# Kernel tuning notes

Hardware: AMD Instinct MI355X
Metric: run time of the kernel (lower is better)

## Reference

```python
import jax, jax.numpy as jnp
import numpy as np

N, C, H, W, D = 4, 320, 16, 16, 16
POS_RATIO = 0.5


def setup_inputs() -> dict:
    key = jax.random.key(0)
    k1, k2, k3, k4 = jax.random.split(key, 4)
    q = jax.random.normal(k1, (N, C, H, W, D), jnp.float32)
    k = jax.random.normal(k2, (N, C, H, W, D), jnp.float32)

    def make_coord(kr):
        # crop boxes: upper-left corner in [0, 0.4), extent in [0.4, 0.6)
        start = jax.random.uniform(kr, (N, 3), jnp.float32) * 0.4
        size = 0.4 + jax.random.uniform(jax.random.fold_in(kr, 1), (N, 3), jnp.float32) * 0.2
        return jnp.concatenate([start, start + size], axis=1)  # (N, 6)

    coord_q = make_coord(k3)
    coord_k = make_coord(k4)
    return {"q": q, "k": k, "coord_q": coord_q, "coord_k": coord_k}


def _centers(coord, h, w, d):
    """coord: (N,6) -> centers (N, h*w*d, 3) of each voxel in global coords, and bin diag (N,)."""
    dims = jnp.array([h, w, d], jnp.float32)
    bin_sz = (coord[:, 3:6] - coord[:, 0:3]) / dims  # (N,3) = (bin_h, bin_w, bin_d)
    ax = jnp.arange(h, dtype=jnp.float32) + 0.5
    ay = jnp.arange(w, dtype=jnp.float32) + 0.5
    az = jnp.arange(d, dtype=jnp.float32) + 0.5
    grid = jnp.stack(jnp.meshgrid(ax, ay, az, indexing="ij"), axis=-1)  # (h,w,d,3)
    grid = grid.reshape(1, h * w * d, 3)
    centers = grid * bin_sz[:, None, :] + coord[:, None, 0:3]  # (N, L, 3)
    diag = jnp.sqrt(jnp.sum(bin_sz ** 2, axis=-1))  # (N,)
    return centers, diag


def reference(q, k, coord_q, coord_k):
    n, c, h, w, d = q.shape
    L = h * w * d
    qf = q.reshape(n, c, L)
    kf = k.reshape(n, c, L)

    cq, diag_q = _centers(coord_q, h, w, d)  # (N,L,3), (N,)
    ck, diag_k = _centers(coord_k, h, w, d)
    max_diag = jnp.maximum(diag_q, diag_k)[:, None, None]  # (N,1,1)

    def masked_loss(q_flat, centers_q):
        # pairwise center distance (N, L, L) -- sum of three squared diffs, no (N,L,L,3) stack
        d2 = ((centers_q[:, :, None, 0] - ck[:, None, :, 0]) ** 2
              + (centers_q[:, :, None, 1] - ck[:, None, :, 1]) ** 2
              + (centers_q[:, :, None, 2] - ck[:, None, :, 2]) ** 2)
        dist = jnp.sqrt(d2) / max_diag
        mask = jax.lax.stop_gradient((dist < POS_RATIO).astype(jnp.float32))
        logit = jnp.einsum("ncl,ncm->nlm", q_flat, kf)  # bmm(q^T, k)
        return jnp.sum(logit * mask, axis=(-2, -1)) / (jnp.sum(mask, axis=(-2, -1)) + 1e-6)

    loss = masked_loss(qf, cq)
    # anatomy branch: flip(q) and flipped q-centers along batch dim 0 (as in source flip(x, dim=0))
    loss_rev = masked_loss(jnp.flip(qf, axis=0), jnp.flip(cq, axis=0))
    return -2.0 * jnp.mean(loss) - 2.0 * jnp.mean(loss_rev)
```

## Files before the change

kernel.cpp:

```cpp
#include <hip/hip_runtime.h>

#define LVOX   4096
#define NCH    320
#define NCOMBO 8
#define NSEG   64
#define SEGCAP 4096
#define PKSTR  17
#define PKROW  (256 * PKSTR)
#define NBLK   (2 * NCH)
#define WPCNT_OFF 2048
#define SPART_OFF 4096
#define RUNS_OFF  24576

struct Geo {
    float qs0, qs1, qs2, qo0, qo1, qo2;
    float ks0, ks1, ks2, ko0, ko1, ko2;
    float ik0, ik1, ik2;
    float T;
};

__device__ __forceinline__ Geo make_geo(const float* __restrict__ cq,
                                        const float* __restrict__ ck,
                                        int n, int qb) {
    Geo g;
    const float* qc = cq + qb * 6;
    const float* qn = cq + n * 6;
    const float* kc = ck + n * 6;
    g.qs0 = (qc[3] - qc[0]) * (1.f / 16.f); g.qo0 = qc[0];
    g.qs1 = (qc[4] - qc[1]) * (1.f / 16.f); g.qo1 = qc[1];
    g.qs2 = (qc[5] - qc[2]) * (1.f / 16.f); g.qo2 = qc[2];
    g.ks0 = (kc[3] - kc[0]) * (1.f / 16.f); g.ko0 = kc[0];
    g.ks1 = (kc[4] - kc[1]) * (1.f / 16.f); g.ko1 = kc[1];
    g.ks2 = (kc[5] - kc[2]) * (1.f / 16.f); g.ko2 = kc[2];
    g.ik0 = 1.f / g.ks0; g.ik1 = 1.f / g.ks1; g.ik2 = 1.f / g.ks2;
    float b0 = (qn[3] - qn[0]) * (1.f / 16.f);
    float b1 = (qn[4] - qn[1]) * (1.f / 16.f);
    float b2 = (qn[5] - qn[2]) * (1.f / 16.f);
    float dq = sqrtf(b0 * b0 + b1 * b1 + b2 * b2);
    float dk = sqrtf(g.ks0 * g.ks0 + g.ks1 * g.ks1 + g.ks2 * g.ks2);
    g.T = 0.5f * fmaxf(dq, dk);
    return g;
}

__device__ __forceinline__ void axrange(float c, float ko, float ik, float T,
                                        int& m0, int& m1) {
    float lo = (c - T - ko) * ik - 0.5f;
    float hi = (c + T - ko) * ik - 0.5f;
    m0 = max((int)ceilf(lo) - 1, 0);
    m1 = min((int)floorf(hi) + 1, 15);
}

__global__ void enum_runs(const float* __restrict__ coord_q,
                          const float* __restrict__ coord_k,
                          unsigned* __restrict__ wcnt,
                          unsigned* __restrict__ wpcnt,
                          unsigned* __restrict__ runs) {
    int gid = blockIdx.x * 256 + threadIdx.x;
    int j = gid >> 12;
    int l = gid & 4095;
    int seg = j * NSEG + ((gid & 4095) >> 6);
    int n = j & 3;
    int qb = (j & 4) ? (3 - n) : n;
    Geo g = make_geo(coord_q, coord_k, n, qb);

    int ix = l >> 8, iy = (l >> 4) & 15, iz = l & 15;
    float cx = (ix + 0.5f) * g.qs0 + g.qo0;
    float cy = (iy + 0.5f) * g.qs1 + g.qo1;
    float cz = (iz + 0.5f) * g.qs2 + g.qo2;
    int x0, x1, y0, y1, z0, z1;
    axrange(cx, g.ko0, g.ik0, g.T, x0, x1);
    axrange(cy, g.ko1, g.ik1, g.T, y0, y1);
    axrange(cz, g.ko2, g.ik2, g.T, z0, z1);

    int nh = 0, nr = 0;
    for (int x = x0; x <= x1; ++x) {
        float dx = cx - ((x + 0.5f) * g.ks0 + g.ko0);
        float dx2 = dx * dx;
        for (int y = y0; y <= y1; ++y) {
            float dy = cy - ((y + 0.5f) * g.ks1 + g.ko1);
            float dxy = dx2 + dy * dy;
            int zc = 0;
            for (int z = z0; z <= z1; ++z) {
                float dz = cz - ((z + 0.5f) * g.ks2 + g.ko2);
                if (sqrtf(dxy + dz * dz) < g.T) zc++;
            }
            if (zc) { nr++; nh += zc; }
        }
    }

    int lane = threadIdx.x & 63;
    int incl = nr;
#pragma unroll
    for (int off = 1; off < 64; off <<= 1) {
        int t = __shfl_up(incl, off, 64);
        if (lane >= off) incl += t;
    }
    int w = incl - nr;
    if (lane == 63) wcnt[seg] = (unsigned)incl;

    int hsum = nh;
#pragma unroll
    for (int off = 32; off; off >>= 1) hsum += __shfl_down(hsum, off, 64);
    if (lane == 0) wpcnt[seg] = (unsigned)hsum;

    unsigned* out = runs + (size_t)seg * SEGCAP;
    for (int x = x0; x <= x1; ++x) {
        float dx = cx - ((x + 0.5f) * g.ks0 + g.ko0);
        float dx2 = dx * dx;
        for (int y = y0; y <= y1; ++y) {
            float dy = cy - ((y + 0.5f) * g.ks1 + g.ko1);
            float dxy = dx2 + dy * dy;
            int zf = -1, zc = 0;
            for (int z = z0; z <= z1; ++z) {
                float dz = cz - ((z + 0.5f) * g.ks2 + g.ko2);
                if (sqrtf(dxy + dz * dz) < g.T) { if (!zc) zf = z; zc++; }
            }
            if (zc) {
                if (w < SEGCAP)
                    out[w] = ((unsigned)l << 16)
                           | ((unsigned)((x << 8) | (y << 4) | zf) << 4)
                           | (unsigned)(zc - 1);
                w++;
            }
        }
    }
}

__global__ void __launch_bounds__(512) gather_fused(
        const float* __restrict__ q, const float* __restrict__ k,
        const unsigned* __restrict__ wcnt, const unsigned* __restrict__ runs,
        float* __restrict__ Spart) {
    __shared__ float sh[2 * LVOX + 2 * PKROW + 32];
    const int QA = 0, QB = LVOX, PK = 2 * LVOX, SR = 2 * LVOX + 2 * PKROW;

    int g = blockIdx.x;
    int c = blockIdx.y;
    int n0 = g ? 1 : 0;
    int n1 = 3 - n0;
    int t = threadIdx.x;

    const float* q0 = q + ((size_t)(n0 * NCH + c)) * LVOX;
    const float* q1 = q + ((size_t)(n1 * NCH + c)) * LVOX;
#pragma unroll
    for (int i = 0; i < 2; ++i) {
        int off = (t + 512 * i) * 4;
        *(float4*)&sh[QA + off] = *(const float4*)&q0[off];
        *(float4*)&sh[QB + off] = *(const float4*)&q1[off];
    }

    {
        int row = t >> 8;
        int cl  = t & 255;
        const float* ks = k + ((size_t)((row ? n1 : n0) * NCH + c)) * LVOX + cl * 16;
        float4 v0 = *(const float4*)&ks[0];
        float4 v1 = *(const float4*)&ks[4];
        float4 v2 = *(const float4*)&ks[8];
        float4 v3 = *(const float4*)&ks[12];
        float vv[16] = {v0.x, v0.y, v0.z, v0.w, v1.x, v1.y, v1.z, v1.w,
                        v2.x, v2.y, v2.z, v2.w, v3.x, v3.y, v3.z, v3.w};
        float* dst = &sh[PK + row * PKROW + cl * PKSTR];
        float e = 0.f;
        dst[0] = 0.f;
#pragma unroll
        for (int i = 0; i < 16; ++i) { e += vv[i]; dst[i + 1] = e; }
    }
    __syncthreads();

    const int jl[4]   = {n0, n1, 4 + n0, 4 + n1};
    const int qoff[4] = {QA, QB, QB, QA};
    const int koff[4] = {PK, PK + PKROW, PK, PK + PKROW};
    float accv[4];

    int segi = t >> 3;
    int tin  = t & 7;

#pragma unroll
    for (int ci = 0; ci < 4; ++ci) {
        int j = jl[ci];
        unsigned cnt = wcnt[j * NSEG + segi];
        if (cnt > SEGCAP) cnt = SEGCAP;
        const unsigned* rl = runs + (size_t)(j * NSEG + segi) * SEGCAP;
        int qb = qoff[ci], kb = koff[ci];
        float acc = 0.f;
        for (unsigned p = (unsigned)tin * 4u; p < cnt; p += 32u) {
            uint4 r4 = *(const uint4*)&rl[p];
            unsigned rr[4] = {r4.x, r4.y, r4.z, r4.w};
#pragma unroll
            for (int e = 0; e < 4; ++e) {
                bool valid = (p + (unsigned)e) < cnt;
                unsigned pr = rr[e];
                int l    = (int)((pr >> 16) & 4095u);
                int cell = (int)((pr >> 8) & 255u);
                int zf   = (int)((pr >> 4) & 15u);
                int len  = (int)(pr & 15u) + 1;
                float s = sh[kb + cell * PKSTR + zf + len] - sh[kb + cell * PKSTR + zf];
                acc += valid ? sh[qb + l] * s : 0.f;
            }
        }
        accv[ci] = acc;
    }

    int wv = t >> 6, lane = t & 63;
#pragma unroll
    for (int ci = 0; ci < 4; ++ci) {
        float a = accv[ci];
#pragma unroll
        for (int off = 32; off; off >>= 1) a += __shfl_down(a, off, 64);
        if (lane == 0) sh[SR + wv * 4 + ci] = a;
    }
    __syncthreads();
    if (t < 4) {
        float v = 0.f;
#pragma unroll
        for (int w = 0; w < 8; ++w) v += sh[SR + w * 4 + t];
        Spart[(size_t)jl[t] * NBLK + (c * 2 + g)] = v;
    }
}

__global__ void finalize(const float* __restrict__ Spart,
                         const unsigned* __restrict__ wpcnt,
                         float* __restrict__ out) {
    __shared__ float tj[NCOMBO];
    int j = threadIdx.x >> 5;
    int s = threadIdx.x & 31;
    int nn = j & 3;
    int gj = (nn == 1 || nn == 2) ? 1 : 0;
    float v = 0.f;
    for (int i = s; i < NCH; i += 32)
        v += Spart[(size_t)j * NBLK + i * 2 + gj];
    unsigned pc = wpcnt[j * NSEG + s] + wpcnt[j * NSEG + s + 32];
    float pcf = (float)pc;
#pragma unroll
    for (int off = 16; off; off >>= 1) {
        v   += __shfl_down(v, off, 32);
        pcf += __shfl_down(pcf, off, 32);
    }
    if (s == 0) tj[j] = v / (pcf + 1e-6f);
    __syncthreads();
    if (threadIdx.x == 0) {
        float t = 0.f;
#pragma unroll
        for (int jj = 0; jj < NCOMBO; ++jj) t += tj[jj];
        out[0] = -0.5f * t;
    }
}

extern "C" void kernel_launch(void* const* d_in, const int* in_sizes, int n_in,
                              void* d_out, int out_size, void* d_ws, size_t ws_size,
                              hipStream_t stream) {
    const float* q       = (const float*)d_in[0];
    const float* k       = (const float*)d_in[1];
    const float* coord_q = (const float*)d_in[2];
    const float* coord_k = (const float*)d_in[3];
    float* out = (float*)d_out;

    unsigned* wcnt  = (unsigned*)d_ws;
    unsigned* wpcnt = (unsigned*)((char*)d_ws + WPCNT_OFF);
    float*    Spart = (float*)((char*)d_ws + SPART_OFF);
    unsigned* runs  = (unsigned*)((char*)d_ws + RUNS_OFF);

    enum_runs<<<(NCOMBO * LVOX) / 256, 256, 0, stream>>>(coord_q, coord_k, wcnt, wpcnt, runs);
    gather_fused<<<dim3(2, NCH), 512, 0, stream>>>(q, k, wcnt, runs, Spart);
    finalize<<<1, 256, 0, stream>>>(Spart, wpcnt, out);
}
```

Before: 124.6 us.

## Pack z-runs two per word with per-voxel headers and offset tables

Replaces the flat one-run-per-word list with a per-voxel layout: a header word holding the voxel index and run count, followed by 16-bit run records packed two per word. Per-lane start offsets are stored so the gather kernel can walk each voxel's runs directly, load the q value once per voxel, and accumulate the k sum before one multiply. This roughly halves the run bytes read per channel block and drops the per-run voxel-index decode. In exchange, SEGCAP shrinks to 1024 with no overflow guard on writes, and the gather loop becomes variable-length per lane, which can diverge.

```diff
diff --git a/kernel.cpp b/kernel.cpp
--- a/kernel.cpp
+++ b/kernel.cpp
@@ -4,13 +4,14 @@
 #define NCH    320
 #define NCOMBO 8
 #define NSEG   64
-#define SEGCAP 4096
+#define SEGCAP 1024
 #define PKSTR  17
 #define PKROW  (256 * PKSTR)
 #define NBLK   (2 * NCH)
-#define WPCNT_OFF 2048
-#define SPART_OFF 4096
-#define RUNS_OFF  24576
+#define GOFFS  65
+#define GOFFX_OFF 2048
+#define SPART_OFF 135168
+#define RUNS_OFF  155648
 
 struct Geo {
     float qs0, qs1, qs2, qo0, qo1, qo2;
@@ -52,8 +53,8 @@
 
 __global__ void enum_runs(const float* __restrict__ coord_q,
                           const float* __restrict__ coord_k,
-                          unsigned* __restrict__ wcnt,
                           unsigned* __restrict__ wpcnt,
+                          unsigned* __restrict__ goffx,
                           unsigned* __restrict__ runs) {
     int gid = blockIdx.x * 256 + threadIdx.x;
     int j = gid >> 12;
@@ -88,47 +89,54 @@
         }
     }
 
+    int wc = nr ? 1 + ((nr + 1) >> 1) : 0;
+
     int lane = threadIdx.x & 63;
-    int incl = nr;
+    int incl = wc;
 #pragma unroll
     for (int off = 1; off < 64; off <<= 1) {
         int t = __shfl_up(incl, off, 64);
         if (lane >= off) incl += t;
     }
-    int w = incl - nr;
-    if (lane == 63) wcnt[seg] = (unsigned)incl;
+    int w = incl - wc;
+    goffx[seg * GOFFS + lane] = (unsigned)w;
+    if (lane == 63) goffx[seg * GOFFS + 64] = (unsigned)incl;
 
     int hsum = nh;
 #pragma unroll
     for (int off = 32; off; off >>= 1) hsum += __shfl_down(hsum, off, 64);
     if (lane == 0) wpcnt[seg] = (unsigned)hsum;
 
-    unsigned* out = runs + (size_t)seg * SEGCAP;
-    for (int x = x0; x <= x1; ++x) {
-        float dx = cx - ((x + 0.5f) * g.ks0 + g.ko0);
-        float dx2 = dx * dx;
-        for (int y = y0; y <= y1; ++y) {
-            float dy = cy - ((y + 0.5f) * g.ks1 + g.ko1);
-            float dxy = dx2 + dy * dy;
-            int zf = -1, zc = 0;
-            for (int z = z0; z <= z1; ++z) {
-                float dz = cz - ((z + 0.5f) * g.ks2 + g.ko2);
-                if (sqrtf(dxy + dz * dz) < g.T) { if (!zc) zf = z; zc++; }
-            }
-            if (zc) {
-                if (w < SEGCAP)
-                    out[w] = ((unsigned)l << 16)
-                           | ((unsigned)((x << 8) | (y << 4) | zf) << 4)
-                           | (unsigned)(zc - 1);
-                w++;
+    if (nr) {
+        unsigned* out = runs + (size_t)seg * SEGCAP;
+        out[w++] = ((unsigned)l << 16) | (unsigned)nr;
+        unsigned pend = 0; int have = 0;
+        for (int x = x0; x <= x1; ++x) {
+            float dx = cx - ((x + 0.5f) * g.ks0 + g.ko0);
+            float dx2 = dx * dx;
+            for (int y = y0; y <= y1; ++y) {
+                float dy = cy - ((y + 0.5f) * g.ks1 + g.ko1);
+                float dxy = dx2 + dy * dy;
+                int zf = -1, zc = 0;
+                for (int z = z0; z <= z1; ++z) {
+                    float dz = cz - ((z + 0.5f) * g.ks2 + g.ko2);
+                    if (sqrtf(dxy + dz * dz) < g.T) { if (!zc) zf = z; zc++; }
+                }
+                if (zc) {
+                    unsigned r = ((unsigned)((x << 4) | y) << 8)
+                               | ((unsigned)zf << 4) | (unsigned)(zc - 1);
+                    if (have) { out[w++] = pend | (r << 16); have = 0; }
+                    else      { pend = r; have = 1; }
+                }
             }
         }
+        if (have) out[w++] = pend;
     }
 }
 
 __global__ void __launch_bounds__(512) gather_fused(
         const float* __restrict__ q, const float* __restrict__ k,
-        const unsigned* __restrict__ wcnt, const unsigned* __restrict__ runs,
+        const unsigned* __restrict__ goffx, const unsigned* __restrict__ runs,
         float* __restrict__ Spart) {
     __shared__ float sh[2 * LVOX + 2 * PKROW + 32];
     const int QA = 0, QB = LVOX, PK = 2 * LVOX, SR = 2 * LVOX + 2 * PKROW;
@@ -177,25 +185,37 @@
 #pragma unroll
     for (int ci = 0; ci < 4; ++ci) {
         int j = jl[ci];
-        unsigned cnt = wcnt[j * NSEG + segi];
-        if (cnt > SEGCAP) cnt = SEGCAP;
-        const unsigned* rl = runs + (size_t)(j * NSEG + segi) * SEGCAP;
+        int seg = j * NSEG + segi;
+        const unsigned* go = goffx + (size_t)seg * GOFFS;
+        const unsigned* rl = runs + (size_t)seg * SEGCAP;
         int qb = qoff[ci], kb = koff[ci];
         float acc = 0.f;
-        for (unsigned p = (unsigned)tin * 4u; p < cnt; p += 32u) {
-            uint4 r4 = *(const uint4*)&rl[p];
-            unsigned rr[4] = {r4.x, r4.y, r4.z, r4.w};
-#pragma unroll
-            for (int e = 0; e < 4; ++e) {
-                bool valid = (p + (unsigned)e) < cnt;
-                unsigned pr = rr[e];
-                int l    = (int)((pr >> 16) & 4095u);
-                int cell = (int)((pr >> 8) & 255u);
-                int zf   = (int)((pr >> 4) & 15u);
-                int len  = (int)(pr & 15u) + 1;
-                float s = sh[kb + cell * PKSTR + zf + len] - sh[kb + cell * PKSTR + zf];
-                acc += valid ? sh[qb + l] * s : 0.f;
+        for (int gi = tin; gi < 64; gi += 8) {
+            unsigned p  = go[gi];
+            unsigned pe = go[gi + 1];
+            if (p >= pe) continue;
+            unsigned h = rl[p++];
+            int l  = (int)((h >> 16) & 4095u);
+            int nr = (int)(h & 255u);
+            float qv = sh[qb + l];
+            float s = 0.f;
+            int nw = (nr + 1) >> 1;
+            for (int wi = 0; wi < nw; ++wi) {
+                unsigned rw = rl[p + wi];
+                unsigned r0 = rw & 0xffffu;
+                int c0 = (int)(r0 >> 8);
+                int z0 = (int)((r0 >> 4) & 15u);
+                int L0 = (int)(r0 & 15u) + 1;
+                s += sh[kb + c0 * PKSTR + z0 + L0] - sh[kb + c0 * PKSTR + z0];
+                if (2 * wi + 1 < nr) {
+                    unsigned r1 = rw >> 16;
+                    int c1 = (int)(r1 >> 8);
+                    int z1 = (int)((r1 >> 4) & 15u);
+                    int L1 = (int)(r1 & 15u) + 1;
+                    s += sh[kb + c1 * PKSTR + z1 + L1] - sh[kb + c1 * PKSTR + z1];
+                }
             }
+            acc += qv * s;
         }
         accv[ci] = acc;
     }
@@ -254,12 +274,12 @@
     const float* coord_k = (const float*)d_in[3];
     float* out = (float*)d_out;
 
-    unsigned* wcnt  = (unsigned*)d_ws;
-    unsigned* wpcnt = (unsigned*)((char*)d_ws + WPCNT_OFF);
+    unsigned* wpcnt = (unsigned*)d_ws;
+    unsigned* goffx = (unsigned*)((char*)d_ws + GOFFX_OFF);
     float*    Spart = (float*)((char*)d_ws + SPART_OFF);
     unsigned* runs  = (unsigned*)((char*)d_ws + RUNS_OFF);
 
-    enum_runs<<<(NCOMBO * LVOX) / 256, 256, 0, stream>>>(coord_q, coord_k, wcnt, wpcnt, runs);
-    gather_fused<<<dim3(2, NCH), 512, 0, stream>>>(q, k, wcnt, runs, Spart);
+    enum_runs<<<(NCOMBO * LVOX) / 256, 256, 0, stream>>>(coord_q, coord_k, wpcnt, goffx, runs);
+    gather_fused<<<dim3(2, NCH), 512, 0, stream>>>(q, k, goffx, runs, Spart);
     finalize<<<1, 256, 0, stream>>>(Spart, wpcnt, out);
 }
```

Measured after the change: 151.2 us. +21.4%, slower.
